# Optimization experiments

Hardware: AMD Instinct MI355X
Metric: run time of the kernel (lower is better)

Reference implementation:

```python
import jax, jax.numpy as jnp
import numpy as np

D = 192   # token_dim == channel_dim == expert_dim == adapt_dim (required by source code)
S = 4096  # sequence length
NE = 8    # num_experts


def _ln(x, g, b, eps=1e-5):
    m = x.mean(-1, keepdims=True)
    v = ((x - m) ** 2).mean(-1, keepdims=True)
    return (x - m) / jnp.sqrt(v + eps) * g + b


def _adaptive(x, a, W, b, AW, Ab):
    # AdaptiveLinear with adapt_method='add': weight = W + adapt(a).view(out, in)
    dW = (AW @ a + Ab).reshape(W.shape)
    return x @ (W + dW).T + b


def setup_inputs() -> dict:
    key = jax.random.key(0)
    ks = iter(jax.random.split(key, 40))

    def n(shape, s=0.05):
        return jax.random.normal(next(ks), shape, dtype=jnp.float32) * s

    return {
        "x": n((1, S, D), 1.0),
        "W_in": n((D, D)), "b_in": n((D,)),
        "feat_W": n((D, D)), "feat_b": n((D,)),
        "feat_AW": n((D * D, D)), "feat_Ab": n((D * D,)),
        "an_g": jnp.ones((D,)), "an_b": jnp.zeros((D,)),
        "tm_W": n((D, D)), "tm_b": n((D,)),
        "tm_AW": n((D * D, D)), "tm_Ab": n((D * D,)),
        "tn_g": jnp.ones((D,)), "tn_b": jnp.zeros((D,)),
        "cm_W": n((D, D)), "cm_b": n((D,)),
        "cm_AW": n((D * D, D)), "cm_Ab": n((D * D,)),
        "cn_g": jnp.ones((D,)), "cn_b": jnp.zeros((D,)),
        "pm_W": n((D, D)), "pm_b": n((D,)),
        "gate_W": n((NE, D)), "gate_b": n((NE,)),
        "ex_W": n((NE, D, D)), "ex_b": n((NE, D)),
        "ex_AW": n((NE, D * D, D)), "ex_Ab": n((NE, D * D)),
        "mn_g": jnp.ones((D,)), "mn_b": jnp.zeros((D,)),
        "out_W": n((D, D)), "out_b": n((D,)),
    }


def reference(x, W_in, b_in, feat_W, feat_b, feat_AW, feat_Ab, an_g, an_b,
              tm_W, tm_b, tm_AW, tm_Ab, tn_g, tn_b,
              cm_W, cm_b, cm_AW, cm_Ab, cn_g, cn_b,
              pm_W, pm_b, gate_W, gate_b, ex_W, ex_b, ex_AW, ex_Ab,
              mn_g, mn_b, out_W, out_b):
    h = x @ W_in.T + b_in                                        # [1,S,D]
    xm = h.mean(axis=1)                                          # [1,D]
    a = _adaptive(xm, xm[0], feat_W, feat_b, feat_AW, feat_Ab)   # [1,D]
    a = _ln(a, an_g, an_b)
    a0 = a[0]                                                    # [D]
    t = _adaptive(h, a0, tm_W, tm_b, tm_AW, tm_Ab)               # token mixing
    t = _ln(t, tn_g, tn_b)
    c = _adaptive(t, a0, cm_W, cm_b, cm_AW, cm_Ab)               # channel mixing
    c = _ln(c, cn_g, cn_b)
    m = c @ pm_W.T + pm_b                                        # pre-MoE [1,S,D]
    gate = jax.nn.softmax(a @ gate_W.T + gate_b, axis=-1)[0]     # [NE]
    # batched hypernet weight generation for all experts at once
    dW = (jnp.einsum('eka,a->ek', ex_AW, a0) + ex_Ab).reshape(NE, D, D)
    We = ex_W + dW                                               # [NE,D,D]
    ye = jnp.einsum('bsd,ned->nbse', m, We) + ex_b[:, None, None, :]
    eo = jnp.einsum('n,nbse->bse', gate, ye)                     # soft-MoE sum
    eo = _ln(eo, mn_g, mn_b)
    eo = jax.nn.relu(eo)
    return eo @ out_W.T + out_b
```

## Files before the change

### kernel.cpp

```cpp
#include <hip/hip_runtime.h>

#define DD 192

template <int EMIT, int LNL>
__global__ __launch_bounds__(256) void stage3_k(
    const float* __restrict__ A, const float* __restrict__ W,
    const float* __restrict__ bias,
    const float* __restrict__ stats_in, const float* __restrict__ lng,
    const float* __restrict__ lnb,
    float* __restrict__ out, float* __restrict__ emit_buf) {
    __shared__ float At[32 * 200];
    __shared__ float WT[DD * 64];
    __shared__ float ms[32], rs[32];
    __shared__ float csum[4 * 64];

    const int t = threadIdx.x;
    const int tr = t >> 5, tc = t & 31;
    const int b = blockIdx.x;
    const int cg = b % 3;
    const int c0 = cg * 64;
    const int r0 = (b / 3) * 32;

    if (LNL > 0) {
        if (t < 32) {
            int r = r0 + t;
            float s = stats_in[2 * r] + stats_in[8192 + 2 * r] + stats_in[16384 + 2 * r];
            float q = stats_in[2 * r + 1] + stats_in[8192 + 2 * r + 1]
                    + stats_in[16384 + 2 * r + 1];
            float mean = s * (1.f / 192.f);
            float var = q * (1.f / 192.f) - mean * mean;
            ms[t] = mean;
            rs[t] = rsqrtf(var + 1e-5f);
        }
        __syncthreads();
    }

    {
        const float4* A4 = (const float4*)(A + (size_t)r0 * DD);
#pragma unroll
        for (int q = 0; q < 6; q++) {
            int f = t + 256 * q;
            int r = f / 48, jj = f - r * 48;
            float4 v = A4[f];
            if (LNL > 0) {
                float mean = ms[r], rstd = rs[r];
                float4 g4 = ((const float4*)lng)[jj];
                float4 b4 = ((const float4*)lnb)[jj];
                v.x = (v.x - mean) * rstd * g4.x + b4.x;
                v.y = (v.y - mean) * rstd * g4.y + b4.y;
                v.z = (v.z - mean) * rstd * g4.z + b4.z;
                v.w = (v.w - mean) * rstd * g4.w + b4.w;
                if (LNL == 2) {
                    v.x = fmaxf(v.x, 0.f); v.y = fmaxf(v.y, 0.f);
                    v.z = fmaxf(v.z, 0.f); v.w = fmaxf(v.w, 0.f);
                }
            }
            *(float4*)&At[r * 200 + 4 * jj] = v;
        }
    }
    {
        const float4* W4 = (const float4*)(W + (size_t)c0 * DD);
#pragma unroll
        for (int q = 0; q < 12; q++) {
            int f = t + 256 * q;
            int ip = f / 48, jj = f - ip * 48;
            float4 v = W4[f];
            int j0 = 4 * jj;
            WT[(j0 + 0) * 64 + ((ip + 2 * ((j0 + 0) & 31)) & 63)] = v.x;
            WT[(j0 + 1) * 64 + ((ip + 2 * ((j0 + 1) & 31)) & 63)] = v.y;
            WT[(j0 + 2) * 64 + ((ip + 2 * ((j0 + 2) & 31)) & 63)] = v.z;
            WT[(j0 + 3) * 64 + ((ip + 2 * ((j0 + 3) & 31)) & 63)] = v.w;
        }
    }

    const int i0 = c0 + 2 * tc;
    float bv0 = bias[i0], bv1 = bias[i0 + 1];
    float acc[4][2];
#pragma unroll
    for (int i = 0; i < 4; i++) { acc[i][0] = bv0; acc[i][1] = bv1; }
    __syncthreads();

    const int rbase = 4 * tr;
#pragma unroll 2
    for (int jc = 0; jc < DD; jc += 8) {
        float a_[4][8];
#pragma unroll
        for (int rr = 0; rr < 4; rr++) {
            float4 u = *(const float4*)&At[(rbase + rr) * 200 + jc];
            float4 v = *(const float4*)&At[(rbase + rr) * 200 + jc + 4];
            a_[rr][0] = u.x; a_[rr][1] = u.y; a_[rr][2] = u.z; a_[rr][3] = u.w;
            a_[rr][4] = v.x; a_[rr][5] = v.y; a_[rr][6] = v.z; a_[rr][7] = v.w;
        }
#pragma unroll
        for (int jj = 0; jj < 8; jj++) {
            const int j = jc + jj;
            int cs = (2 * tc + 2 * (j & 31)) & 63;
            float2 w2 = *(const float2*)&WT[j * 64 + cs];
            acc[0][0] = fmaf(a_[0][jj], w2.x, acc[0][0]);
            acc[0][1] = fmaf(a_[0][jj], w2.y, acc[0][1]);
            acc[1][0] = fmaf(a_[1][jj], w2.x, acc[1][0]);
            acc[1][1] = fmaf(a_[1][jj], w2.y, acc[1][1]);
            acc[2][0] = fmaf(a_[2][jj], w2.x, acc[2][0]);
            acc[2][1] = fmaf(a_[2][jj], w2.y, acc[2][1]);
            acc[3][0] = fmaf(a_[3][jj], w2.x, acc[3][0]);
            acc[3][1] = fmaf(a_[3][jj], w2.y, acc[3][1]);
        }
    }

#pragma unroll
    for (int i = 0; i < 4; i++) {
        int row = r0 + rbase + i;
        *(float2*)&out[(size_t)row * DD + i0] = make_float2(acc[i][0], acc[i][1]);
    }

    if (EMIT == 2) {
#pragma unroll
        for (int i = 0; i < 4; i++) {
            float s = acc[i][0] + acc[i][1];
            float q = acc[i][0] * acc[i][0] + acc[i][1] * acc[i][1];
#pragma unroll
            for (int m = 16; m >= 1; m >>= 1) {
                s += __shfl_xor(s, m);
                q += __shfl_xor(q, m);
            }
            if (tc == 0) {
                int r = r0 + rbase + i;
                emit_buf[cg * 8192 + 2 * r] = s;
                emit_buf[cg * 8192 + 2 * r + 1] = q;
            }
        }
    } else if (EMIT == 1) {
        float cs0 = acc[0][0] + acc[1][0] + acc[2][0] + acc[3][0];
        float cs1 = acc[0][1] + acc[1][1] + acc[2][1] + acc[3][1];
        cs0 += __shfl_xor(cs0, 32);
        cs1 += __shfl_xor(cs1, 32);
        int w = t >> 6;
        if ((t & 63) < 32) {
            csum[w * 64 + 2 * tc] = cs0;
            csum[w * 64 + 2 * tc + 1] = cs1;
        }
        __syncthreads();
        if (t < 64) {
            float s = csum[t] + csum[64 + t] + csum[128 + t] + csum[192 + t];
            atomicAdd(&emit_buf[c0 + t], s);
        }
    }
}

__global__ __launch_bounds__(256) void hyper_k(
    const float* __restrict__ tm_W, const float* __restrict__ tm_AW,
    const float* __restrict__ tm_Ab, const float* __restrict__ cm_W,
    const float* __restrict__ cm_AW, const float* __restrict__ cm_Ab,
    const float* __restrict__ ex_W, const float* __restrict__ ex_AW,
    const float* __restrict__ ex_Ab, const float* __restrict__ a0g,
    const float* __restrict__ gateg, float* __restrict__ Wt,
    float* __restrict__ Wc, float* __restrict__ Wmoe) {
    __shared__ float a0s[DD];
    __shared__ float rows[32 * 204];
    __shared__ float wb[32], ab[32], vals[32];
    __shared__ float gs[8];
    const int t = threadIdx.x;
    const int b = blockIdx.x;
    const int r = t >> 3, p = t & 7;
    if (t < DD) a0s[t] = a0g[t];

    if (b < 2304) {
        const float* AW; const float* WB; const float* AB; float* dst;
        int k0;
        if (b < 1152) { AW = tm_AW; WB = tm_W; AB = tm_Ab; dst = Wt; k0 = b * 32; }
        else          { AW = cm_AW; WB = cm_W; AB = cm_Ab; dst = Wc; k0 = (b - 1152) * 32; }
        if (t < 32) { wb[t] = WB[k0 + t]; ab[t] = AB[k0 + t]; }
        const float4* src4 = (const float4*)(AW + (size_t)k0 * DD);
#pragma unroll
        for (int q = 0; q < 6; q++) {
            int fidx = t + 256 * q;
            int rr = fidx / 48, jj = fidx - rr * 48;
            *(float4*)&rows[rr * 204 + 4 * jj] = src4[fidx];
        }
        __syncthreads();
        float acc = 0.f;
#pragma unroll
        for (int q = 0; q < 6; q++) {
            int jo = p * 24 + 4 * q;
            float4 w = *(const float4*)&rows[r * 204 + jo];
            float4 aa = *(const float4*)&a0s[jo];
            acc = fmaf(w.x, aa.x, acc); acc = fmaf(w.y, aa.y, acc);
            acc = fmaf(w.z, aa.z, acc); acc = fmaf(w.w, aa.w, acc);
        }
        acc += __shfl_xor(acc, 1);
        acc += __shfl_xor(acc, 2);
        acc += __shfl_xor(acc, 4);
        if (p == 0) vals[r] = acc + wb[r] + ab[r];
        __syncthreads();
        if (t < 32) dst[k0 + t] = vals[t];
    } else {
        const int k0 = (b - 2304) * 32;
        if (t < 8) gs[t] = gateg[t];
        float macc = 0.f;
        for (int e = 0; e < 8; e++) {
            __syncthreads();
            const float4* src4 =
                (const float4*)(ex_AW + (size_t)e * 36864 * DD + (size_t)k0 * DD);
#pragma unroll
            for (int q = 0; q < 6; q++) {
                int fidx = t + 256 * q;
                int rr = fidx / 48, jj = fidx - rr * 48;
                *(float4*)&rows[rr * 204 + 4 * jj] = src4[fidx];
            }
            __syncthreads();
            float acc = 0.f;
#pragma unroll
            for (int q = 0; q < 6; q++) {
                int jo = p * 24 + 4 * q;
                float4 w = *(const float4*)&rows[r * 204 + jo];
                float4 aa = *(const float4*)&a0s[jo];
                acc = fmaf(w.x, aa.x, acc); acc = fmaf(w.y, aa.y, acc);
                acc = fmaf(w.z, aa.z, acc); acc = fmaf(w.w, aa.w, acc);
            }
            acc += __shfl_xor(acc, 1);
            acc += __shfl_xor(acc, 2);
            acc += __shfl_xor(acc, 4);
            if (p == 0) vals[r] = acc;
            __syncthreads();
            if (t < 32) {
                float we = ex_W[(size_t)e * 36864 + k0 + t];
                float ae = ex_Ab[(size_t)e * 36864 + k0 + t];
                macc = fmaf(gs[e], vals[t] + we + ae, macc);
            }
        }
        if (t < 32) Wmoe[k0 + t] = macc;
    }
}

__global__ __launch_bounds__(256) void feat2_k(
    const float* __restrict__ feat_W, const float* __restrict__ feat_AW,
    const float* __restrict__ feat_Ab, const float* __restrict__ xm_sum,
    float* __restrict__ a_pre) {
    __shared__ float xms[DD];
    __shared__ float rows[32 * 204];
    __shared__ float wb[32], ab[32], vals[32];
    const int t = threadIdx.x;
    const int k0 = blockIdx.x * 32;
    if (t < DD) xms[t] = xm_sum[t] * (1.f / 4096.f);
    if (t < 32) { wb[t] = feat_W[k0 + t]; ab[t] = feat_Ab[k0 + t]; }
    const float4* src4 = (const float4*)(feat_AW + (size_t)k0 * DD);
#pragma unroll
    for (int q = 0; q < 6; q++) {
        int fidx = t + 256 * q;
        int r = fidx / 48, jj = fidx - r * 48;
        float4 v = src4[fidx];
        *(float4*)&rows[r * 204 + 4 * jj] = v;
    }
    __syncthreads();
    const int r = t >> 3, p = t & 7;
    float acc = 0.f;
#pragma unroll
    for (int q = 0; q < 6; q++) {
        int jo = p * 24 + 4 * q;
        float4 w = *(const float4*)&rows[r * 204 + jo];
        float4 aa = *(const float4*)&xms[jo];
        acc = fmaf(w.x, aa.x, acc); acc = fmaf(w.y, aa.y, acc);
        acc = fmaf(w.z, aa.z, acc); acc = fmaf(w.w, aa.w, acc);
    }
    acc += __shfl_xor(acc, 1);
    acc += __shfl_xor(acc, 2);
    acc += __shfl_xor(acc, 4);
    if (p == 0) vals[r] = acc + wb[r] + ab[r];
    __syncthreads();
    const int j0 = k0 % DD;
    if (t < 32) {
        float c = vals[t] * xms[j0 + t];
#pragma unroll
        for (int m = 16; m >= 1; m >>= 1) c += __shfl_xor(c, m);
        if (t == 0) atomicAdd(&a_pre[k0 / DD], c);
    }
}

__global__ __launch_bounds__(192) void vec_k(
    const float* __restrict__ a_pre, const float* __restrict__ feat_b,
    const float* __restrict__ an_g, const float* __restrict__ an_b,
    const float* __restrict__ gate_W, const float* __restrict__ gate_b,
    const float* __restrict__ ex_b, float* __restrict__ a0g,
    float* __restrict__ gateg, float* __restrict__ b_moe) {
    __shared__ float red[6];
    __shared__ float gred[24];
    __shared__ float lgs[8];
    const int t = threadIdx.x;
    const int w = t >> 6;
    float v = a_pre[t] + feat_b[t];
    float s = v, q = v * v;
#pragma unroll
    for (int m = 32; m >= 1; m >>= 1) {
        s += __shfl_xor(s, m);
        q += __shfl_xor(q, m);
    }
    if ((t & 63) == 0) { red[w] = s; red[3 + w] = q; }
    __syncthreads();
    float S = red[0] + red[1] + red[2];
    float Q = red[3] + red[4] + red[5];
    float mean = S * (1.f / 192.f);
    float var = Q * (1.f / 192.f) - mean * mean;
    float rstd = rsqrtf(var + 1e-5f);
    float a0v = (v - mean) * rstd * an_g[t] + an_b[t];
    a0g[t] = a0v;
#pragma unroll
    for (int e = 0; e < 8; e++) {
        float x = a0v * gate_W[e * DD + t];
#pragma unroll
        for (int m = 32; m >= 1; m >>= 1) x += __shfl_xor(x, m);
        if ((t & 63) == 0) gred[w * 8 + e] = x;
    }
    __syncthreads();
    if (t < 8) lgs[t] = gred[t] + gred[8 + t] + gred[16 + t] + gate_b[t];
    __syncthreads();
    if (t == 0) {
        float mx = lgs[0];
        for (int e = 1; e < 8; e++) mx = fmaxf(mx, lgs[e]);
        float sum = 0.f, ex[8];
        for (int e = 0; e < 8; e++) { ex[e] = expf(lgs[e] - mx); sum += ex[e]; }
        for (int e = 0; e < 8; e++) lgs[e] = ex[e] / sum;
    }
    __syncthreads();
    if (t < 8) gateg[t] = lgs[t];
    float bm = 0.f;
#pragma unroll
    for (int e = 0; e < 8; e++) bm = fmaf(lgs[e], ex_b[e * DD + t], bm);
    b_moe[t] = bm;
}

extern "C" void kernel_launch(void* const* d_in, const int* in_sizes, int n_in,
                              void* d_out, int out_size, void* d_ws, size_t ws_size,
                              hipStream_t stream) {
    (void)in_sizes; (void)n_in; (void)out_size; (void)ws_size;
    const float* x       = (const float*)d_in[0];
    const float* W_in    = (const float*)d_in[1];
    const float* b_in    = (const float*)d_in[2];
    const float* feat_W  = (const float*)d_in[3];
    const float* feat_b  = (const float*)d_in[4];
    const float* feat_AW = (const float*)d_in[5];
    const float* feat_Ab = (const float*)d_in[6];
    const float* an_g    = (const float*)d_in[7];
    const float* an_b    = (const float*)d_in[8];
    const float* tm_W    = (const float*)d_in[9];
    const float* tm_b    = (const float*)d_in[10];
    const float* tm_AW   = (const float*)d_in[11];
    const float* tm_Ab   = (const float*)d_in[12];
    const float* tn_g    = (const float*)d_in[13];
    const float* tn_b    = (const float*)d_in[14];
    const float* cm_W    = (const float*)d_in[15];
    const float* cm_b    = (const float*)d_in[16];
    const float* cm_AW   = (const float*)d_in[17];
    const float* cm_Ab   = (const float*)d_in[18];
    const float* cn_g    = (const float*)d_in[19];
    const float* cn_b    = (const float*)d_in[20];
    const float* pm_W    = (const float*)d_in[21];
    const float* pm_b    = (const float*)d_in[22];
    const float* gate_W  = (const float*)d_in[23];
    const float* gate_b  = (const float*)d_in[24];
    const float* ex_W    = (const float*)d_in[25];
    const float* ex_b    = (const float*)d_in[26];
    const float* ex_AW   = (const float*)d_in[27];
    const float* ex_Ab   = (const float*)d_in[28];
    const float* mn_g    = (const float*)d_in[29];
    const float* mn_b    = (const float*)d_in[30];
    const float* out_W   = (const float*)d_in[31];
    const float* out_b   = (const float*)d_in[32];

    float* ws = (float*)d_ws;
    float* B0     = ws;
    float* B1     = ws + 786432;
    float* xm_sum = ws + 1572864;
    float* a_pre  = ws + 1573056;
    float* Wmoe   = ws + 1573248;
    float* Wt     = ws + 1610112;
    float* Wc     = ws + 1646976;
    float* st1    = ws + 1683840;
    float* st2    = ws + 1708416;
    float* st3    = ws + 1732992;
    float* a0     = ws + 1757568;
    float* gate   = ws + 1757760;
    float* b_moe  = ws + 1757768;

    hipMemsetAsync(xm_sum, 0, (size_t)384 * sizeof(float), stream);

    stage3_k<1, 0><<<384, 256, 0, stream>>>(x, W_in, b_in, nullptr, nullptr, nullptr,
                                            B0, xm_sum);
    feat2_k<<<1152, 256, 0, stream>>>(feat_W, feat_AW, feat_Ab, xm_sum, a_pre);
    vec_k<<<1, 192, 0, stream>>>(a_pre, feat_b, an_g, an_b, gate_W, gate_b, ex_b,
                                 a0, gate, b_moe);
    hyper_k<<<3456, 256, 0, stream>>>(tm_W, tm_AW, tm_Ab, cm_W, cm_AW, cm_Ab,
                                      ex_W, ex_AW, ex_Ab, a0, gate, Wt, Wc, Wmoe);
    stage3_k<2, 0><<<384, 256, 0, stream>>>(B0, Wt, tm_b, nullptr, nullptr, nullptr,
                                            B1, st1);
    stage3_k<2, 1><<<384, 256, 0, stream>>>(B1, Wc, cm_b, st1, tn_g, tn_b, B0, st2);
    stage3_k<0, 1><<<384, 256, 0, stream>>>(B0, pm_W, pm_b, st2, cn_g, cn_b, B1, nullptr);
    stage3_k<2, 0><<<384, 256, 0, stream>>>(B1, Wmoe, b_moe, nullptr, nullptr, nullptr,
                                            B0, st3);
    stage3_k<0, 2><<<384, 256, 0, stream>>>(B0, out_W, out_b, st3, mn_g, mn_b,
                                            (float*)d_out, nullptr);
}
```

Before: 532.5 us.

## Fuse all stages into one cooperative persistent kernel with grid syncs

Replaces the chain of separate kernel launches with a single cooperative kernel of 384 blocks that runs every phase (transpose, input projection, feature hypernet, vector ops, weight generation, five GEMM stages) and separates them with grid-wide barriers. Hypernet outputs and the static weights are written transposed to global memory, so the GEMM stages stream weights from global into registers with a one-step prefetch instead of staging them in shared memory. The goal is to remove launch gaps and the shared-memory weight staging. In exchange, grid syncs add barrier cost, the hypernet phases run with fewer blocks looping over their chunks, and a fallback path of separate launches is kept for when cooperative launch fails.

```diff
diff --git a/kernel.cpp b/kernel.cpp
--- a/kernel.cpp
+++ b/kernel.cpp
@@ -1,25 +1,53 @@
 #include <hip/hip_runtime.h>
+#include <hip/hip_cooperative_groups.h>
 
 #define DD 192
 
+namespace cg = cooperative_groups;
+
+
+struct KParams {
+    const float *x, *W_in, *b_in, *feat_W, *feat_b, *feat_AW, *feat_Ab, *an_g, *an_b;
+    const float *tm_W, *tm_b, *tm_AW, *tm_Ab, *tn_g, *tn_b;
+    const float *cm_W, *cm_b, *cm_AW, *cm_Ab, *cn_g, *cn_b;
+    const float *pm_W, *pm_b, *gate_W, *gate_b;
+    const float *ex_W, *ex_b, *ex_AW, *ex_Ab, *mn_g, *mn_b, *out_W, *out_b;
+    float *B0, *B1, *xm_sum, *a_pre, *WmoeT, *WtT, *WcT, *st1, *st2, *st3;
+    float *a0, *gate, *b_moe, *WinT, *pmT, *outT, *out;
+};
+
+struct Smem {
+    float big[32 * 204];
+    float aux[DD];
+    float ms[32], rs[32];
+    float csum[256];
+    float wb[32], ab[32], vals[32], gs[8];
+    float red[6], gred[24], lgs[8];
+};
+
+__device__ __forceinline__ void transpose3(const KParams& P) {
+    int g = blockIdx.x * 256 + threadIdx.x;
+    const int N = 36864;
+    for (; g < 3 * N; g += 384 * 256) {
+        int m = g / N, e = g - m * N;
+        int i = e / DD, j = e - i * DD;
+        const float* src = (m == 0) ? P.W_in : (m == 1) ? P.pm_W : P.out_W;
+        float* dst = (m == 0) ? P.WinT : (m == 1) ? P.pmT : P.outT;
+        dst[(size_t)j * DD + i] = src[e];
+    }
+}
+
 template <int EMIT, int LNL>
-__global__ __launch_bounds__(256) void stage3_k(
-    const float* __restrict__ A, const float* __restrict__ W,
-    const float* __restrict__ bias,
-    const float* __restrict__ stats_in, const float* __restrict__ lng,
-    const float* __restrict__ lnb,
-    float* __restrict__ out, float* __restrict__ emit_buf) {
-    __shared__ float At[32 * 200];
-    __shared__ float WT[DD * 64];
-    __shared__ float ms[32], rs[32];
-    __shared__ float csum[4 * 64];
-
+__device__ __forceinline__ void stage3_phase(
+    const float* A, const float* WTg, const float* bias,
+    const float* stats_in, const float* lng, const float* lnb,
+    float* out, float* emit_buf, Smem& S) {
     const int t = threadIdx.x;
     const int tr = t >> 5, tc = t & 31;
     const int b = blockIdx.x;
-    const int cg = b % 3;
-    const int c0 = cg * 64;
+    const int cg = b % 3, c0 = cg * 64;
     const int r0 = (b / 3) * 32;
+    float* At = S.big;
 
     if (LNL > 0) {
         if (t < 32) {
@@ -29,12 +57,11 @@
                     + stats_in[16384 + 2 * r + 1];
             float mean = s * (1.f / 192.f);
             float var = q * (1.f / 192.f) - mean * mean;
-            ms[t] = mean;
-            rs[t] = rsqrtf(var + 1e-5f);
+            S.ms[t] = mean;
+            S.rs[t] = rsqrtf(var + 1e-5f);
         }
         __syncthreads();
     }
-
     {
         const float4* A4 = (const float4*)(A + (size_t)r0 * DD);
 #pragma unroll
@@ -43,7 +70,7 @@
             int r = f / 48, jj = f - r * 48;
             float4 v = A4[f];
             if (LNL > 0) {
-                float mean = ms[r], rstd = rs[r];
+                float mean = S.ms[r], rstd = S.rs[r];
                 float4 g4 = ((const float4*)lng)[jj];
                 float4 b4 = ((const float4*)lnb)[jj];
                 v.x = (v.x - mean) * rstd * g4.x + b4.x;
@@ -58,31 +85,26 @@
             *(float4*)&At[r * 200 + 4 * jj] = v;
         }
     }
-    {
-        const float4* W4 = (const float4*)(W + (size_t)c0 * DD);
-#pragma unroll
-        for (int q = 0; q < 12; q++) {
-            int f = t + 256 * q;
-            int ip = f / 48, jj = f - ip * 48;
-            float4 v = W4[f];
-            int j0 = 4 * jj;
-            WT[(j0 + 0) * 64 + ((ip + 2 * ((j0 + 0) & 31)) & 63)] = v.x;
-            WT[(j0 + 1) * 64 + ((ip + 2 * ((j0 + 1) & 31)) & 63)] = v.y;
-            WT[(j0 + 2) * 64 + ((ip + 2 * ((j0 + 2) & 31)) & 63)] = v.z;
-            WT[(j0 + 3) * 64 + ((ip + 2 * ((j0 + 3) & 31)) & 63)] = v.w;
-        }
-    }
-
     const int i0 = c0 + 2 * tc;
+    const float* wp = WTg + i0;
     float bv0 = bias[i0], bv1 = bias[i0 + 1];
     float acc[4][2];
 #pragma unroll
     for (int i = 0; i < 4; i++) { acc[i][0] = bv0; acc[i][1] = bv1; }
+    float2 wreg[8];
+#pragma unroll
+    for (int jj = 0; jj < 8; jj++) wreg[jj] = *(const float2*)(wp + jj * DD);
     __syncthreads();
 
     const int rbase = 4 * tr;
 #pragma unroll 2
-    for (int jc = 0; jc < DD; jc += 8) {
+    for (int jc = 0; jc < DD - 8; jc += 8) {
+        float2 wcur[8];
+#pragma unroll
+        for (int jj = 0; jj < 8; jj++) wcur[jj] = wreg[jj];
+#pragma unroll
+        for (int jj = 0; jj < 8; jj++)
+            wreg[jj] = *(const float2*)(wp + (jc + 8 + jj) * DD);
         float a_[4][8];
 #pragma unroll
         for (int rr = 0; rr < 4; rr++) {
@@ -93,17 +115,36 @@
         }
 #pragma unroll
         for (int jj = 0; jj < 8; jj++) {
-            const int j = jc + jj;
-            int cs = (2 * tc + 2 * (j & 31)) & 63;
-            float2 w2 = *(const float2*)&WT[j * 64 + cs];
-            acc[0][0] = fmaf(a_[0][jj], w2.x, acc[0][0]);
-            acc[0][1] = fmaf(a_[0][jj], w2.y, acc[0][1]);
-            acc[1][0] = fmaf(a_[1][jj], w2.x, acc[1][0]);
-            acc[1][1] = fmaf(a_[1][jj], w2.y, acc[1][1]);
-            acc[2][0] = fmaf(a_[2][jj], w2.x, acc[2][0]);
-            acc[2][1] = fmaf(a_[2][jj], w2.y, acc[2][1]);
-            acc[3][0] = fmaf(a_[3][jj], w2.x, acc[3][0]);
-            acc[3][1] = fmaf(a_[3][jj], w2.y, acc[3][1]);
+            acc[0][0] = fmaf(a_[0][jj], wcur[jj].x, acc[0][0]);
+            acc[0][1] = fmaf(a_[0][jj], wcur[jj].y, acc[0][1]);
+            acc[1][0] = fmaf(a_[1][jj], wcur[jj].x, acc[1][0]);
+            acc[1][1] = fmaf(a_[1][jj], wcur[jj].y, acc[1][1]);
+            acc[2][0] = fmaf(a_[2][jj], wcur[jj].x, acc[2][0]);
+            acc[2][1] = fmaf(a_[2][jj], wcur[jj].y, acc[2][1]);
+            acc[3][0] = fmaf(a_[3][jj], wcur[jj].x, acc[3][0]);
+            acc[3][1] = fmaf(a_[3][jj], wcur[jj].y, acc[3][1]);
+        }
+    }
+    {
+        const int jc = DD - 8;
+        float a_[4][8];
+#pragma unroll
+        for (int rr = 0; rr < 4; rr++) {
+            float4 u = *(const float4*)&At[(rbase + rr) * 200 + jc];
+            float4 v = *(const float4*)&At[(rbase + rr) * 200 + jc + 4];
+            a_[rr][0] = u.x; a_[rr][1] = u.y; a_[rr][2] = u.z; a_[rr][3] = u.w;
+            a_[rr][4] = v.x; a_[rr][5] = v.y; a_[rr][6] = v.z; a_[rr][7] = v.w;
+        }
+#pragma unroll
+        for (int jj = 0; jj < 8; jj++) {
+            acc[0][0] = fmaf(a_[0][jj], wreg[jj].x, acc[0][0]);
+            acc[0][1] = fmaf(a_[0][jj], wreg[jj].y, acc[0][1]);
+            acc[1][0] = fmaf(a_[1][jj], wreg[jj].x, acc[1][0]);
+            acc[1][1] = fmaf(a_[1][jj], wreg[jj].y, acc[1][1]);
+            acc[2][0] = fmaf(a_[2][jj], wreg[jj].x, acc[2][0]);
+            acc[2][1] = fmaf(a_[2][jj], wreg[jj].y, acc[2][1]);
+            acc[3][0] = fmaf(a_[3][jj], wreg[jj].x, acc[3][0]);
+            acc[3][1] = fmaf(a_[3][jj], wreg[jj].y, acc[3][1]);
         }
     }
 
@@ -136,46 +177,33 @@
         cs1 += __shfl_xor(cs1, 32);
         int w = t >> 6;
         if ((t & 63) < 32) {
-            csum[w * 64 + 2 * tc] = cs0;
-            csum[w * 64 + 2 * tc + 1] = cs1;
+            S.csum[w * 64 + 2 * tc] = cs0;
+            S.csum[w * 64 + 2 * tc + 1] = cs1;
         }
         __syncthreads();
         if (t < 64) {
-            float s = csum[t] + csum[64 + t] + csum[128 + t] + csum[192 + t];
+            float s = S.csum[t] + S.csum[64 + t] + S.csum[128 + t] + S.csum[192 + t];
             atomicAdd(&emit_buf[c0 + t], s);
         }
     }
 }
 
-__global__ __launch_bounds__(256) void hyper_k(
-    const float* __restrict__ tm_W, const float* __restrict__ tm_AW,
-    const float* __restrict__ tm_Ab, const float* __restrict__ cm_W,
-    const float* __restrict__ cm_AW, const float* __restrict__ cm_Ab,
-    const float* __restrict__ ex_W, const float* __restrict__ ex_AW,
-    const float* __restrict__ ex_Ab, const float* __restrict__ a0g,
-    const float* __restrict__ gateg, float* __restrict__ Wt,
-    float* __restrict__ Wc, float* __restrict__ Wmoe) {
-    __shared__ float a0s[DD];
-    __shared__ float rows[32 * 204];
-    __shared__ float wb[32], ab[32], vals[32];
-    __shared__ float gs[8];
+__device__ __forceinline__ void feat2_phase(const KParams& P, Smem& S) {
     const int t = threadIdx.x;
-    const int b = blockIdx.x;
+    float* rows = S.big;
+    if (t < DD) S.aux[t] = P.xm_sum[t] * (1.f / 4096.f);
     const int r = t >> 3, p = t & 7;
-    if (t < DD) a0s[t] = a0g[t];
-
-    if (b < 2304) {
-        const float* AW; const float* WB; const float* AB; float* dst;
-        int k0;
-        if (b < 1152) { AW = tm_AW; WB = tm_W; AB = tm_Ab; dst = Wt; k0 = b * 32; }
-        else          { AW = cm_AW; WB = cm_W; AB = cm_Ab; dst = Wc; k0 = (b - 1152) * 32; }
-        if (t < 32) { wb[t] = WB[k0 + t]; ab[t] = AB[k0 + t]; }
-        const float4* src4 = (const float4*)(AW + (size_t)k0 * DD);
+    for (int q3 = 0; q3 < 3; q3++) {
+        const int c = blockIdx.x + 384 * q3;
+        const int k0 = c * 32;
+        __syncthreads();
+        if (t < 32) { S.wb[t] = P.feat_W[k0 + t]; S.ab[t] = P.feat_Ab[k0 + t]; }
+        const float4* src4 = (const float4*)(P.feat_AW + (size_t)k0 * DD);
 #pragma unroll
         for (int q = 0; q < 6; q++) {
-            int fidx = t + 256 * q;
-            int rr = fidx / 48, jj = fidx - rr * 48;
-            *(float4*)&rows[rr * 204 + 4 * jj] = src4[fidx];
+            int f = t + 256 * q;
+            int rr = f / 48, jj = f - rr * 48;
+            *(float4*)&rows[rr * 204 + 4 * jj] = src4[f];
         }
         __syncthreads();
         float acc = 0.f;
@@ -183,29 +211,92 @@
         for (int q = 0; q < 6; q++) {
             int jo = p * 24 + 4 * q;
             float4 w = *(const float4*)&rows[r * 204 + jo];
-            float4 aa = *(const float4*)&a0s[jo];
+            float4 aa = *(const float4*)&S.aux[jo];
             acc = fmaf(w.x, aa.x, acc); acc = fmaf(w.y, aa.y, acc);
             acc = fmaf(w.z, aa.z, acc); acc = fmaf(w.w, aa.w, acc);
         }
         acc += __shfl_xor(acc, 1);
         acc += __shfl_xor(acc, 2);
         acc += __shfl_xor(acc, 4);
-        if (p == 0) vals[r] = acc + wb[r] + ab[r];
+        if (p == 0) S.vals[r] = acc + S.wb[r] + S.ab[r];
         __syncthreads();
-        if (t < 32) dst[k0 + t] = vals[t];
-    } else {
-        const int k0 = (b - 2304) * 32;
-        if (t < 8) gs[t] = gateg[t];
-        float macc = 0.f;
-        for (int e = 0; e < 8; e++) {
+        const int j0 = k0 % DD;
+        if (t < 32) {
+            float cp = S.vals[t] * S.aux[j0 + t];
+#pragma unroll
+            for (int m = 16; m >= 1; m >>= 1) cp += __shfl_xor(cp, m);
+            if (t == 0) atomicAdd(&P.a_pre[k0 / DD], cp);
+        }
+    }
+}
+
+__device__ __forceinline__ void vec_phase(const KParams& P, Smem& S) {
+    const int t = threadIdx.x;
+    const int w = t >> 6;
+    float v = (t < DD) ? (P.a_pre[t] + P.feat_b[t]) : 0.f;
+    float s = v, q = v * v;
+#pragma unroll
+    for (int m = 32; m >= 1; m >>= 1) { s += __shfl_xor(s, m); q += __shfl_xor(q, m); }
+    if (((t & 63) == 0) && w < 3) { S.red[w] = s; S.red[3 + w] = q; }
+    __syncthreads();
+    float a0v = 0.f;
+    if (t < DD) {
+        float Ssum = S.red[0] + S.red[1] + S.red[2];
+        float Q = S.red[3] + S.red[4] + S.red[5];
+        float mean = Ssum * (1.f / 192.f);
+        float var = Q * (1.f / 192.f) - mean * mean;
+        float rstd = rsqrtf(var + 1e-5f);
+        a0v = (v - mean) * rstd * P.an_g[t] + P.an_b[t];
+        P.a0[t] = a0v;
+    }
+#pragma unroll
+    for (int e = 0; e < 8; e++) {
+        float xv = (t < DD) ? a0v * P.gate_W[e * DD + t] : 0.f;
+#pragma unroll
+        for (int m = 32; m >= 1; m >>= 1) xv += __shfl_xor(xv, m);
+        if (((t & 63) == 0) && w < 3) S.gred[w * 8 + e] = xv;
+    }
+    __syncthreads();
+    if (t < 8) S.lgs[t] = S.gred[t] + S.gred[8 + t] + S.gred[16 + t] + P.gate_b[t];
+    __syncthreads();
+    if (t == 0) {
+        float mx = S.lgs[0];
+        for (int e = 1; e < 8; e++) mx = fmaxf(mx, S.lgs[e]);
+        float sum = 0.f, ex[8];
+        for (int e = 0; e < 8; e++) { ex[e] = expf(S.lgs[e] - mx); sum += ex[e]; }
+        for (int e = 0; e < 8; e++) S.lgs[e] = ex[e] / sum;
+    }
+    __syncthreads();
+    if (t < 8) P.gate[t] = S.lgs[t];
+    if (t < DD) {
+        float bm = 0.f;
+#pragma unroll
+        for (int e = 0; e < 8; e++) bm = fmaf(S.lgs[e], P.ex_b[e * DD + t], bm);
+        P.b_moe[t] = bm;
+    }
+}
+
+__device__ __forceinline__ void hyper_phase(const KParams& P, Smem& S) {
+    const int t = threadIdx.x;
+    float* rows = S.big;
+    if (t < DD) S.aux[t] = P.a0[t];
+    if (t < 8) S.gs[t] = P.gate[t];
+    const int r = t >> 3, p = t & 7;
+    for (int q9 = 0; q9 < 9; q9++) {
+        const int c = blockIdx.x + 384 * q9;
+        if (c < 2304) {
+            const float* AW; const float* WB; const float* AB; float* dstT;
+            int k0;
+            if (c < 1152) { AW = P.tm_AW; WB = P.tm_W; AB = P.tm_Ab; dstT = P.WtT; k0 = c * 32; }
+            else { AW = P.cm_AW; WB = P.cm_W; AB = P.cm_Ab; dstT = P.WcT; k0 = (c - 1152) * 32; }
             __syncthreads();
-            const float4* src4 =
-                (const float4*)(ex_AW + (size_t)e * 36864 * DD + (size_t)k0 * DD);
+            if (t < 32) { S.wb[t] = WB[k0 + t]; S.ab[t] = AB[k0 + t]; }
+            const float4* src4 = (const float4*)(AW + (size_t)k0 * DD);
 #pragma unroll
             for (int q = 0; q < 6; q++) {
-                int fidx = t + 256 * q;
-                int rr = fidx / 48, jj = fidx - rr * 48;
-                *(float4*)&rows[rr * 204 + 4 * jj] = src4[fidx];
+                int f = t + 256 * q;
+                int rr = f / 48, jj = f - rr * 48;
+                *(float4*)&rows[rr * 204 + 4 * jj] = src4[f];
             }
             __syncthreads();
             float acc = 0.f;
@@ -213,189 +304,188 @@
             for (int q = 0; q < 6; q++) {
                 int jo = p * 24 + 4 * q;
                 float4 w = *(const float4*)&rows[r * 204 + jo];
-                float4 aa = *(const float4*)&a0s[jo];
+                float4 aa = *(const float4*)&S.aux[jo];
                 acc = fmaf(w.x, aa.x, acc); acc = fmaf(w.y, aa.y, acc);
                 acc = fmaf(w.z, aa.z, acc); acc = fmaf(w.w, aa.w, acc);
             }
             acc += __shfl_xor(acc, 1);
             acc += __shfl_xor(acc, 2);
             acc += __shfl_xor(acc, 4);
-            if (p == 0) vals[r] = acc;
+            if (p == 0) S.vals[r] = acc + S.wb[r] + S.ab[r];
             __syncthreads();
             if (t < 32) {
-                float we = ex_W[(size_t)e * 36864 + k0 + t];
-                float ae = ex_Ab[(size_t)e * 36864 + k0 + t];
-                macc = fmaf(gs[e], vals[t] + we + ae, macc);
-            }
-        }
-        if (t < 32) Wmoe[k0 + t] = macc;
-    }
-}
-
-__global__ __launch_bounds__(256) void feat2_k(
-    const float* __restrict__ feat_W, const float* __restrict__ feat_AW,
-    const float* __restrict__ feat_Ab, const float* __restrict__ xm_sum,
-    float* __restrict__ a_pre) {
-    __shared__ float xms[DD];
-    __shared__ float rows[32 * 204];
-    __shared__ float wb[32], ab[32], vals[32];
-    const int t = threadIdx.x;
-    const int k0 = blockIdx.x * 32;
-    if (t < DD) xms[t] = xm_sum[t] * (1.f / 4096.f);
-    if (t < 32) { wb[t] = feat_W[k0 + t]; ab[t] = feat_Ab[k0 + t]; }
-    const float4* src4 = (const float4*)(feat_AW + (size_t)k0 * DD);
-#pragma unroll
-    for (int q = 0; q < 6; q++) {
-        int fidx = t + 256 * q;
-        int r = fidx / 48, jj = fidx - r * 48;
-        float4 v = src4[fidx];
-        *(float4*)&rows[r * 204 + 4 * jj] = v;
-    }
-    __syncthreads();
-    const int r = t >> 3, p = t & 7;
-    float acc = 0.f;
-#pragma unroll
-    for (int q = 0; q < 6; q++) {
-        int jo = p * 24 + 4 * q;
-        float4 w = *(const float4*)&rows[r * 204 + jo];
-        float4 aa = *(const float4*)&xms[jo];
-        acc = fmaf(w.x, aa.x, acc); acc = fmaf(w.y, aa.y, acc);
-        acc = fmaf(w.z, aa.z, acc); acc = fmaf(w.w, aa.w, acc);
-    }
-    acc += __shfl_xor(acc, 1);
-    acc += __shfl_xor(acc, 2);
-    acc += __shfl_xor(acc, 4);
-    if (p == 0) vals[r] = acc + wb[r] + ab[r];
-    __syncthreads();
-    const int j0 = k0 % DD;
-    if (t < 32) {
-        float c = vals[t] * xms[j0 + t];
-#pragma unroll
-        for (int m = 16; m >= 1; m >>= 1) c += __shfl_xor(c, m);
-        if (t == 0) atomicAdd(&a_pre[k0 / DD], c);
-    }
-}
-
-__global__ __launch_bounds__(192) void vec_k(
-    const float* __restrict__ a_pre, const float* __restrict__ feat_b,
-    const float* __restrict__ an_g, const float* __restrict__ an_b,
-    const float* __restrict__ gate_W, const float* __restrict__ gate_b,
-    const float* __restrict__ ex_b, float* __restrict__ a0g,
-    float* __restrict__ gateg, float* __restrict__ b_moe) {
-    __shared__ float red[6];
-    __shared__ float gred[24];
-    __shared__ float lgs[8];
-    const int t = threadIdx.x;
-    const int w = t >> 6;
-    float v = a_pre[t] + feat_b[t];
-    float s = v, q = v * v;
-#pragma unroll
-    for (int m = 32; m >= 1; m >>= 1) {
-        s += __shfl_xor(s, m);
-        q += __shfl_xor(q, m);
-    }
-    if ((t & 63) == 0) { red[w] = s; red[3 + w] = q; }
-    __syncthreads();
-    float S = red[0] + red[1] + red[2];
-    float Q = red[3] + red[4] + red[5];
-    float mean = S * (1.f / 192.f);
-    float var = Q * (1.f / 192.f) - mean * mean;
-    float rstd = rsqrtf(var + 1e-5f);
-    float a0v = (v - mean) * rstd * an_g[t] + an_b[t];
-    a0g[t] = a0v;
-#pragma unroll
-    for (int e = 0; e < 8; e++) {
-        float x = a0v * gate_W[e * DD + t];
-#pragma unroll
-        for (int m = 32; m >= 1; m >>= 1) x += __shfl_xor(x, m);
-        if ((t & 63) == 0) gred[w * 8 + e] = x;
-    }
-    __syncthreads();
-    if (t < 8) lgs[t] = gred[t] + gred[8 + t] + gred[16 + t] + gate_b[t];
-    __syncthreads();
-    if (t == 0) {
-        float mx = lgs[0];
-        for (int e = 1; e < 8; e++) mx = fmaxf(mx, lgs[e]);
-        float sum = 0.f, ex[8];
-        for (int e = 0; e < 8; e++) { ex[e] = expf(lgs[e] - mx); sum += ex[e]; }
-        for (int e = 0; e < 8; e++) lgs[e] = ex[e] / sum;
-    }
-    __syncthreads();
-    if (t < 8) gateg[t] = lgs[t];
-    float bm = 0.f;
-#pragma unroll
-    for (int e = 0; e < 8; e++) bm = fmaf(lgs[e], ex_b[e * DD + t], bm);
-    b_moe[t] = bm;
+                int i = k0 / DD, j = k0 - i * DD + t;
+                dstT[(size_t)j * DD + i] = S.vals[t];
+            }
+        } else {
+            const int k0 = (c - 2304) * 32;
+            float macc = 0.f;
+            for (int e = 0; e < 8; e++) {
+                __syncthreads();
+                const float4* src4 =
+                    (const float4*)(P.ex_AW + (size_t)e * 36864 * DD + (size_t)k0 * DD);
+#pragma unroll
+                for (int q = 0; q < 6; q++) {
+                    int f = t + 256 * q;
+                    int rr = f / 48, jj = f - rr * 48;
+                    *(float4*)&rows[rr * 204 + 4 * jj] = src4[f];
+                }
+                __syncthreads();
+                float acc = 0.f;
+#pragma unroll
+                for (int q = 0; q < 6; q++) {
+                    int jo = p * 24 + 4 * q;
+                    float4 w = *(const float4*)&rows[r * 204 + jo];
+                    float4 aa = *(const float4*)&S.aux[jo];
+                    acc = fmaf(w.x, aa.x, acc); acc = fmaf(w.y, aa.y, acc);
+                    acc = fmaf(w.z, aa.z, acc); acc = fmaf(w.w, aa.w, acc);
+                }
+                acc += __shfl_xor(acc, 1);
+                acc += __shfl_xor(acc, 2);
+                acc += __shfl_xor(acc, 4);
+                if (p == 0) S.vals[r] = acc;
+                __syncthreads();
+                if (t < 32) {
+                    float we = P.ex_W[(size_t)e * 36864 + k0 + t];
+                    float ae = P.ex_Ab[(size_t)e * 36864 + k0 + t];
+                    macc = fmaf(S.gs[e], S.vals[t] + we + ae, macc);
+                }
+            }
+            if (t < 32) {
+                int i = k0 / DD, j = k0 - i * DD + t;
+                P.WmoeT[(size_t)j * DD + i] = macc;
+            }
+        }
+    }
+}
+
+__global__ __launch_bounds__(256, 2) void fused_k(KParams P) {
+    cg::grid_group grid = cg::this_grid();
+    __shared__ Smem S;
+    transpose3(P);
+    grid.sync();
+    stage3_phase<1, 0>(P.x, P.WinT, P.b_in, nullptr, nullptr, nullptr, P.B0, P.xm_sum, S);
+    grid.sync();
+    feat2_phase(P, S);
+    grid.sync();
+    if (blockIdx.x == 0) vec_phase(P, S);
+    grid.sync();
+    hyper_phase(P, S);
+    grid.sync();
+    stage3_phase<2, 0>(P.B0, P.WtT, P.tm_b, nullptr, nullptr, nullptr, P.B1, P.st1, S);
+    grid.sync();
+    stage3_phase<2, 1>(P.B1, P.WcT, P.cm_b, P.st1, P.tn_g, P.tn_b, P.B0, P.st2, S);
+    grid.sync();
+    stage3_phase<0, 1>(P.B0, P.pmT, P.pm_b, P.st2, P.cn_g, P.cn_b, P.B1, nullptr, S);
+    grid.sync();
+    stage3_phase<2, 0>(P.B1, P.WmoeT, P.b_moe, nullptr, nullptr, nullptr, P.B0, P.st3, S);
+    grid.sync();
+    stage3_phase<0, 2>(P.B0, P.outT, P.out_b, P.st3, P.mn_g, P.mn_b, P.out, nullptr, S);
+}
+
+__global__ __launch_bounds__(256, 2) void ph_tr_k(KParams P) { transpose3(P); }
+__global__ __launch_bounds__(256, 2) void ph_s1_k(KParams P) {
+    __shared__ Smem S;
+    stage3_phase<1, 0>(P.x, P.WinT, P.b_in, nullptr, nullptr, nullptr, P.B0, P.xm_sum, S);
+}
+__global__ __launch_bounds__(256, 2) void ph_f2_k(KParams P) { __shared__ Smem S; feat2_phase(P, S); }
+__global__ __launch_bounds__(256, 2) void ph_vec_k(KParams P) { __shared__ Smem S; vec_phase(P, S); }
+__global__ __launch_bounds__(256, 2) void ph_hy_k(KParams P) { __shared__ Smem S; hyper_phase(P, S); }
+__global__ __launch_bounds__(256, 2) void ph_s2_k(KParams P) {
+    __shared__ Smem S;
+    stage3_phase<2, 0>(P.B0, P.WtT, P.tm_b, nullptr, nullptr, nullptr, P.B1, P.st1, S);
+}
+__global__ __launch_bounds__(256, 2) void ph_s3_k(KParams P) {
+    __shared__ Smem S;
+    stage3_phase<2, 1>(P.B1, P.WcT, P.cm_b, P.st1, P.tn_g, P.tn_b, P.B0, P.st2, S);
+}
+__global__ __launch_bounds__(256, 2) void ph_s4_k(KParams P) {
+    __shared__ Smem S;
+    stage3_phase<0, 1>(P.B0, P.pmT, P.pm_b, P.st2, P.cn_g, P.cn_b, P.B1, nullptr, S);
+}
+__global__ __launch_bounds__(256, 2) void ph_s5_k(KParams P) {
+    __shared__ Smem S;
+    stage3_phase<2, 0>(P.B1, P.WmoeT, P.b_moe, nullptr, nullptr, nullptr, P.B0, P.st3, S);
+}
+__global__ __launch_bounds__(256, 2) void ph_s6_k(KParams P) {
+    __shared__ Smem S;
+    stage3_phase<0, 2>(P.B0, P.outT, P.out_b, P.st3, P.mn_g, P.mn_b, P.out, nullptr, S);
 }
 
 extern "C" void kernel_launch(void* const* d_in, const int* in_sizes, int n_in,
                               void* d_out, int out_size, void* d_ws, size_t ws_size,
                               hipStream_t stream) {
     (void)in_sizes; (void)n_in; (void)out_size; (void)ws_size;
-    const float* x       = (const float*)d_in[0];
-    const float* W_in    = (const float*)d_in[1];
-    const float* b_in    = (const float*)d_in[2];
-    const float* feat_W  = (const float*)d_in[3];
-    const float* feat_b  = (const float*)d_in[4];
-    const float* feat_AW = (const float*)d_in[5];
-    const float* feat_Ab = (const float*)d_in[6];
-    const float* an_g    = (const float*)d_in[7];
-    const float* an_b    = (const float*)d_in[8];
-    const float* tm_W    = (const float*)d_in[9];
-    const float* tm_b    = (const float*)d_in[10];
-    const float* tm_AW   = (const float*)d_in[11];
-    const float* tm_Ab   = (const float*)d_in[12];
-    const float* tn_g    = (const float*)d_in[13];
-    const float* tn_b    = (const float*)d_in[14];
-    const float* cm_W    = (const float*)d_in[15];
-    const float* cm_b    = (const float*)d_in[16];
-    const float* cm_AW   = (const float*)d_in[17];
-    const float* cm_Ab   = (const float*)d_in[18];
-    const float* cn_g    = (const float*)d_in[19];
-    const float* cn_b    = (const float*)d_in[20];
-    const float* pm_W    = (const float*)d_in[21];
-    const float* pm_b    = (const float*)d_in[22];
-    const float* gate_W  = (const float*)d_in[23];
-    const float* gate_b  = (const float*)d_in[24];
-    const float* ex_W    = (const float*)d_in[25];
-    const float* ex_b    = (const float*)d_in[26];
-    const float* ex_AW   = (const float*)d_in[27];
-    const float* ex_Ab   = (const float*)d_in[28];
-    const float* mn_g    = (const float*)d_in[29];
-    const float* mn_b    = (const float*)d_in[30];
-    const float* out_W   = (const float*)d_in[31];
-    const float* out_b   = (const float*)d_in[32];
-
     float* ws = (float*)d_ws;
-    float* B0     = ws;
-    float* B1     = ws + 786432;
-    float* xm_sum = ws + 1572864;
-    float* a_pre  = ws + 1573056;
-    float* Wmoe   = ws + 1573248;
-    float* Wt     = ws + 1610112;
-    float* Wc     = ws + 1646976;
-    float* st1    = ws + 1683840;
-    float* st2    = ws + 1708416;
-    float* st3    = ws + 1732992;
-    float* a0     = ws + 1757568;
-    float* gate   = ws + 1757760;
-    float* b_moe  = ws + 1757768;
-
-    hipMemsetAsync(xm_sum, 0, (size_t)384 * sizeof(float), stream);
-
-    stage3_k<1, 0><<<384, 256, 0, stream>>>(x, W_in, b_in, nullptr, nullptr, nullptr,
-                                            B0, xm_sum);
-    feat2_k<<<1152, 256, 0, stream>>>(feat_W, feat_AW, feat_Ab, xm_sum, a_pre);
-    vec_k<<<1, 192, 0, stream>>>(a_pre, feat_b, an_g, an_b, gate_W, gate_b, ex_b,
-                                 a0, gate, b_moe);
-    hyper_k<<<3456, 256, 0, stream>>>(tm_W, tm_AW, tm_Ab, cm_W, cm_AW, cm_Ab,
-                                      ex_W, ex_AW, ex_Ab, a0, gate, Wt, Wc, Wmoe);
-    stage3_k<2, 0><<<384, 256, 0, stream>>>(B0, Wt, tm_b, nullptr, nullptr, nullptr,
-                                            B1, st1);
-    stage3_k<2, 1><<<384, 256, 0, stream>>>(B1, Wc, cm_b, st1, tn_g, tn_b, B0, st2);
-    stage3_k<0, 1><<<384, 256, 0, stream>>>(B0, pm_W, pm_b, st2, cn_g, cn_b, B1, nullptr);
-    stage3_k<2, 0><<<384, 256, 0, stream>>>(B1, Wmoe, b_moe, nullptr, nullptr, nullptr,
-                                            B0, st3);
-    stage3_k<0, 2><<<384, 256, 0, stream>>>(B0, out_W, out_b, st3, mn_g, mn_b,
-                                            (float*)d_out, nullptr);
-}
+
+    KParams P;
+    P.x       = (const float*)d_in[0];
+    P.W_in    = (const float*)d_in[1];
+    P.b_in    = (const float*)d_in[2];
+    P.feat_W  = (const float*)d_in[3];
+    P.feat_b  = (const float*)d_in[4];
+    P.feat_AW = (const float*)d_in[5];
+    P.feat_Ab = (const float*)d_in[6];
+    P.an_g    = (const float*)d_in[7];
+    P.an_b    = (const float*)d_in[8];
+    P.tm_W    = (const float*)d_in[9];
+    P.tm_b    = (const float*)d_in[10];
+    P.tm_AW   = (const float*)d_in[11];
+    P.tm_Ab   = (const float*)d_in[12];
+    P.tn_g    = (const float*)d_in[13];
+    P.tn_b    = (const float*)d_in[14];
+    P.cm_W    = (const float*)d_in[15];
+    P.cm_b    = (const float*)d_in[16];
+    P.cm_AW   = (const float*)d_in[17];
+    P.cm_Ab   = (const float*)d_in[18];
+    P.cn_g    = (const float*)d_in[19];
+    P.cn_b    = (const float*)d_in[20];
+    P.pm_W    = (const float*)d_in[21];
+    P.pm_b    = (const float*)d_in[22];
+    P.gate_W  = (const float*)d_in[23];
+    P.gate_b  = (const float*)d_in[24];
+    P.ex_W    = (const float*)d_in[25];
+    P.ex_b    = (const float*)d_in[26];
+    P.ex_AW   = (const float*)d_in[27];
+    P.ex_Ab   = (const float*)d_in[28];
+    P.mn_g    = (const float*)d_in[29];
+    P.mn_b    = (const float*)d_in[30];
+    P.out_W   = (const float*)d_in[31];
+    P.out_b   = (const float*)d_in[32];
+
+    P.B0     = ws;
+    P.B1     = ws + 786432;
+    P.xm_sum = ws + 1572864;
+    P.a_pre  = ws + 1573056;
+    P.WmoeT  = ws + 1573248;
+    P.WtT    = ws + 1610112;
+    P.WcT    = ws + 1646976;
+    P.st1    = ws + 1683840;
+    P.st2    = ws + 1708416;
+    P.st3    = ws + 1732992;
+    P.a0     = ws + 1757568;
+    P.gate   = ws + 1757760;
+    P.b_moe  = ws + 1757768;
+    P.WinT   = ws + 1758208;
+    P.pmT    = ws + 1795072;
+    P.outT   = ws + 1831936;
+    P.out    = (float*)d_out;
+
+    hipMemsetAsync(P.xm_sum, 0, (size_t)384 * sizeof(float), stream);
+
+    void* args[] = { (void*)&P };
+    hipError_t err = hipLaunchCooperativeKernel((void*)fused_k, dim3(384), dim3(256),
+                                                args, 0, stream);
+    if (err != hipSuccess) {
+        ph_tr_k<<<384, 256, 0, stream>>>(P);
+        ph_s1_k<<<384, 256, 0, stream>>>(P);
+        ph_f2_k<<<384, 256, 0, stream>>>(P);
+        ph_vec_k<<<1, 256, 0, stream>>>(P);
+        ph_hy_k<<<384, 256, 0, stream>>>(P);
+        ph_s2_k<<<384, 256, 0, stream>>>(P);
+        ph_s3_k<<<384, 256, 0, stream>>>(P);
+        ph_s4_k<<<384, 256, 0, stream>>>(P);
+        ph_s5_k<<<384, 256, 0, stream>>>(P);
+        ph_s6_k<<<384, 256, 0, stream>>>(P);
+    }
+}
```

Measured after the change: 1.025 ms. 92.5% more time.
